# Kernel tuning notes

Measured on AMD Instinct MI355X. Metric: run time of the kernel, lower is better.

Reference implementation:

```python
import jax, jax.numpy as jnp
import numpy as np

B, N, E = 1024, 4096, 16384
MAX_COL_W, ROW_W = 4, 8


def setup_inputs() -> dict:
    key = jax.random.key(0)
    k1, k2, k3, k4, k5 = jax.random.split(key, 5)
    return {
        "channelLLR": jax.random.normal(k1, (B, N), dtype=jnp.float32),
        "e2oLLR": jax.random.normal(k2, (B, E), dtype=jnp.float32),
        "maxColWeight": MAX_COL_W,
        "edgeToVar": jax.random.randint(k3, (B, N, MAX_COL_W), 0, E, dtype=jnp.int32),
        "edgeToVarMask": jnp.ones((B, N, MAX_COL_W), dtype=jnp.float32),
        "oddToEven": jax.random.randint(k4, (B, E), 0, N, dtype=jnp.int32),
        "edgeToChk": jax.random.randint(k5, (B, E, ROW_W - 1), 0, E, dtype=jnp.int32),
        "rowWeight": ROW_W,
        "alpha": jnp.ones((1,), dtype=jnp.float32),
    }


def reference(channelLLR, e2oLLR, maxColWeight, edgeToVar, edgeToVarMask,
              oddToEven, edgeToChk, rowWeight, alpha):
    b = channelLLR.shape[0]
    # variable-node update: gather incoming edge messages, mask, sum
    msgToVars = jnp.take_along_axis(e2oLLR, edgeToVar.reshape(b, -1), axis=1)
    msgToVars = msgToVars.reshape(b, -1, maxColWeight) * edgeToVarMask  # [B,N,colW]
    llr = channelLLR + jnp.sum(msgToVars, axis=2)                      # [B,N]
    # extrinsic variable-to-check message per edge
    llr = jnp.take_along_axis(llr, oddToEven, axis=1) - e2oLLR         # [B,E]
    # check-node min-sum update over rowWeight-1 peer edges
    msgToChecks = jnp.take_along_axis(llr, edgeToChk.reshape(b, -1), axis=1)
    msgToChecks = msgToChecks.reshape(b, -1, rowWeight - 1)            # [B,E,rowW-1]
    mn = jnp.min(jnp.abs(msgToChecks), axis=2)                         # [B,E]
    sign = jnp.prod(jnp.sign(msgToChecks), axis=2)                     # [B,E]
    e2o = sign * (mn * alpha[0])                                       # [B,E]
    # marginalized posterior LLR per variable node
    out = jnp.take_along_axis(e2o, edgeToVar.reshape(b, -1), axis=1)
    out = out.reshape(b, -1, maxColWeight) * edgeToVarMask
    out = channelLLR + jnp.sum(out, axis=2)                            # [B,N]
    return (out, e2o)
```

## Files before the change

kernel.cpp:

```cpp
#include <hip/hip_runtime.h>

#define BB   1024
#define NN   4096
#define EE   16384
#define COLW 4
#define ROWW1 7
#define TPB  512
#define NWAVE (TPB / 64)
#define GRP_DW (64 * ROWW1)
#define NIT  (EE / TPB)

__global__ __launch_bounds__(TPB, 4) void msl_fused_kernel(
    const float* __restrict__ channelLLR,
    const float* __restrict__ e2oLLR,
    const int*   __restrict__ edgeToVar,
    const float* __restrict__ edgeToVarMask,
    const int*   __restrict__ oddToEven,
    const int*   __restrict__ edgeToChk,
    const float* __restrict__ alpha,
    float*       __restrict__ out,
    float*       __restrict__ e2o_out)
{
    __shared__ __align__(16) float scr_lds[NN];
    __shared__ __align__(16) float edge_lds[EE];
    const int b    = blockIdx.x;
    const int tid  = threadIdx.x;
    const int wave = tid >> 6;
    const int lane = tid & 63;
    const float alph = alpha[0];

    {
        const float4* __restrict__ src = reinterpret_cast<const float4*>(e2oLLR + (size_t)b * EE);
        float4* dst = reinterpret_cast<float4*>(edge_lds);
        #pragma unroll
        for (int k = 0; k < EE / 4 / TPB; ++k) {
            int i = tid + k * TPB;
            dst[i] = src[i];
        }
    }
    __syncthreads();

    uint2  idxpk[NN / TPB];
    float4 mreg[NN / TPB];
    {
        const int4*   __restrict__ ev4 = reinterpret_cast<const int4*>(edgeToVar + (size_t)b * NN * COLW);
        const float4* __restrict__ mk4 = reinterpret_cast<const float4*>(edgeToVarMask + (size_t)b * NN * COLW);
        const float*  __restrict__ chrow = channelLLR + (size_t)b * NN;
        #pragma unroll
        for (int k = 0; k < NN / TPB; ++k) {
            int n = tid + k * TPB;
            int4  idx = ev4[n];
            float4 m  = mk4[n];
            float acc = chrow[n];
            acc += edge_lds[idx.x] * m.x;
            acc += edge_lds[idx.y] * m.y;
            acc += edge_lds[idx.z] * m.z;
            acc += edge_lds[idx.w] * m.w;
            scr_lds[n] = acc;
            idxpk[k] = make_uint2((unsigned)idx.x | ((unsigned)idx.y << 16),
                                  (unsigned)idx.z | ((unsigned)idx.w << 16));
            mreg[k] = m;
        }
    }
    __syncthreads();

    {
        const int* __restrict__ o2erow = oddToEven + (size_t)b * EE;
        #pragma unroll 8
        for (int k = 0; k < NIT; ++k) {
            int e = tid + k * TPB;
            edge_lds[e] = scr_lds[o2erow[e]] - edge_lds[e];
        }
    }
    __syncthreads();

    float e2oreg[NIT];
    {
        const int* __restrict__ ecrow = edgeToChk + (size_t)b * (size_t)EE * ROWW1;
        float* __restrict__ e2orow = e2o_out + (size_t)b * EE;
        float* __restrict__ scratch = scr_lds + wave * GRP_DW;
        int idx[ROWW1];
        {
            const int* __restrict__ p = ecrow + (size_t)wave * GRP_DW + lane;
            #pragma unroll
            for (int j = 0; j < ROWW1; ++j) idx[j] = p[64 * j];
        }
        #pragma unroll
        for (int it = 0; it < NIT; ++it) {
            const int g = it * NWAVE + wave;
            __builtin_amdgcn_wave_barrier();
            asm volatile("s_waitcnt lgkmcnt(0)" ::: "memory");
            __builtin_amdgcn_wave_barrier();
            #pragma unroll
            for (int j = 0; j < ROWW1; ++j) scratch[lane + 64 * j] = edge_lds[idx[j]];
            if (it + 1 < NIT) {
                const int* __restrict__ p = ecrow + (size_t)(g + NWAVE) * GRP_DW + lane;
                #pragma unroll
                for (int j = 0; j < ROWW1; ++j) idx[j] = p[64 * j];
            }
            __builtin_amdgcn_wave_barrier();
            asm volatile("s_waitcnt lgkmcnt(0)" ::: "memory");
            __builtin_amdgcn_wave_barrier();
            float mn = 3.0e38f;
            unsigned sgn = 0u;
            const float* __restrict__ sb = scratch + lane * ROWW1;
            #pragma unroll
            for (int j = 0; j < ROWW1; ++j) {
                float u = sb[j];
                sgn ^= __float_as_uint(u);
                mn = fminf(mn, fabsf(u));
            }
            float val = mn * alph;
            float r = __uint_as_float(__float_as_uint(val) ^ (sgn & 0x80000000u));
            e2oreg[it] = r;
            e2orow[64 * g + lane] = r;
        }
    }
    __syncthreads();

    #pragma unroll
    for (int k = 0; k < NIT; ++k) {
        edge_lds[tid + k * TPB] = e2oreg[k];
    }
    __syncthreads();

    {
        float* __restrict__ outrow = out + (size_t)b * NN;
        const float* __restrict__ chrow = channelLLR + (size_t)b * NN;
        #pragma unroll
        for (int k = 0; k < NN / TPB; ++k) {
            int n = tid + k * TPB;
            uint2  pk = idxpk[k];
            float4 m  = mreg[k];
            float acc = chrow[n];
            acc += edge_lds[pk.x & 0xFFFFu] * m.x;
            acc += edge_lds[pk.x >> 16]     * m.y;
            acc += edge_lds[pk.y & 0xFFFFu] * m.z;
            acc += edge_lds[pk.y >> 16]     * m.w;
            outrow[n] = acc;
        }
    }
}

extern "C" void kernel_launch(void* const* d_in, const int* in_sizes, int n_in,
                              void* d_out, int out_size, void* d_ws, size_t ws_size,
                              hipStream_t stream) {
    const float* channelLLR    = (const float*)d_in[0];
    const float* e2oLLR        = (const float*)d_in[1];
    const int*   edgeToVar     = (const int*)d_in[3];
    const float* edgeToVarMask = (const float*)d_in[4];
    const int*   oddToEven     = (const int*)d_in[5];
    const int*   edgeToChk     = (const int*)d_in[6];
    const float* alpha         = (const float*)d_in[8];

    float* out     = (float*)d_out;
    float* e2o_out = (float*)d_out + (size_t)BB * NN;

    msl_fused_kernel<<<BB, TPB, 0, stream>>>(
        channelLLR, e2oLLR, edgeToVar, edgeToVarMask,
        oddToEven, edgeToChk, alpha, out, e2o_out);
}
```

Before: 180.6 us.

## Double block size, stage e2o in separate LDS buffer and write it coalesced

Block size doubles to 1024 threads. A dedicated LDS buffer now holds the check-node outputs, so the register staging and one barrier pass are removed, and e2o is written to global memory as float4 at the end. Edge indices and channel LLRs stay unpacked in registers, so the posterior pass skips the global re-read and the unpacking. LDS use rises to about 156 KB per block, which limits residency to one block per CU and leaves less room to hide barrier stalls.

New measurement: 164.4 us. -9.0%, faster.

```diff
diff --git a/kernel.cpp b/kernel.cpp
--- a/kernel.cpp
+++ b/kernel.cpp
@@ -5,12 +5,13 @@
 #define EE   16384
 #define COLW 4
 #define ROWW1 7
-#define TPB  512
+#define TPB  1024
 #define NWAVE (TPB / 64)
 #define GRP_DW (64 * ROWW1)
+#define SCR_DW (NWAVE * GRP_DW)
 #define NIT  (EE / TPB)
 
-__global__ __launch_bounds__(TPB, 4) void msl_fused_kernel(
+__global__ __launch_bounds__(TPB) void msl_fused_kernel(
     const float* __restrict__ channelLLR,
     const float* __restrict__ e2oLLR,
     const int*   __restrict__ edgeToVar,
@@ -21,8 +22,9 @@
     float*       __restrict__ out,
     float*       __restrict__ e2o_out)
 {
-    __shared__ __align__(16) float scr_lds[NN];
     __shared__ __align__(16) float edge_lds[EE];
+    __shared__ __align__(16) float e2o_lds[EE];
+    __shared__ __align__(16) float scr_lds[SCR_DW];
     const int b    = blockIdx.x;
     const int tid  = threadIdx.x;
     const int wave = tid >> 6;
@@ -40,8 +42,9 @@
     }
     __syncthreads();
 
-    uint2  idxpk[NN / TPB];
+    int4   idxreg[NN / TPB];
     float4 mreg[NN / TPB];
+    float  chreg[NN / TPB];
     {
         const int4*   __restrict__ ev4 = reinterpret_cast<const int4*>(edgeToVar + (size_t)b * NN * COLW);
         const float4* __restrict__ mk4 = reinterpret_cast<const float4*>(edgeToVarMask + (size_t)b * NN * COLW);
@@ -51,15 +54,14 @@
             int n = tid + k * TPB;
             int4  idx = ev4[n];
             float4 m  = mk4[n];
-            float acc = chrow[n];
+            float ch  = chrow[n];
+            float acc = ch;
             acc += edge_lds[idx.x] * m.x;
             acc += edge_lds[idx.y] * m.y;
             acc += edge_lds[idx.z] * m.z;
             acc += edge_lds[idx.w] * m.w;
             scr_lds[n] = acc;
-            idxpk[k] = make_uint2((unsigned)idx.x | ((unsigned)idx.y << 16),
-                                  (unsigned)idx.z | ((unsigned)idx.w << 16));
-            mreg[k] = m;
+            idxreg[k] = idx; mreg[k] = m; chreg[k] = ch;
         }
     }
     __syncthreads();
@@ -74,10 +76,8 @@
     }
     __syncthreads();
 
-    float e2oreg[NIT];
     {
         const int* __restrict__ ecrow = edgeToChk + (size_t)b * (size_t)EE * ROWW1;
-        float* __restrict__ e2orow = e2o_out + (size_t)b * EE;
         float* __restrict__ scratch = scr_lds + wave * GRP_DW;
         int idx[ROWW1];
         {
@@ -112,32 +112,35 @@
             }
             float val = mn * alph;
             float r = __uint_as_float(__float_as_uint(val) ^ (sgn & 0x80000000u));
-            e2oreg[it] = r;
-            e2orow[64 * g + lane] = r;
+            e2o_lds[64 * g + lane] = r;
         }
     }
-    __syncthreads();
 
-    #pragma unroll
-    for (int k = 0; k < NIT; ++k) {
-        edge_lds[tid + k * TPB] = e2oreg[k];
-    }
-    __syncthreads();
+    asm volatile("s_waitcnt lgkmcnt(0)\n\ts_barrier" ::: "memory");
 
     {
         float* __restrict__ outrow = out + (size_t)b * NN;
-        const float* __restrict__ chrow = channelLLR + (size_t)b * NN;
         #pragma unroll
         for (int k = 0; k < NN / TPB; ++k) {
             int n = tid + k * TPB;
-            uint2  pk = idxpk[k];
+            int4  idx = idxreg[k];
             float4 m  = mreg[k];
-            float acc = chrow[n];
-            acc += edge_lds[pk.x & 0xFFFFu] * m.x;
-            acc += edge_lds[pk.x >> 16]     * m.y;
-            acc += edge_lds[pk.y & 0xFFFFu] * m.z;
-            acc += edge_lds[pk.y >> 16]     * m.w;
+            float acc = chreg[k];
+            acc += e2o_lds[idx.x] * m.x;
+            acc += e2o_lds[idx.y] * m.y;
+            acc += e2o_lds[idx.z] * m.z;
+            acc += e2o_lds[idx.w] * m.w;
             outrow[n] = acc;
+        }
+    }
+
+    {
+        const float4* __restrict__ src = reinterpret_cast<const float4*>(e2o_lds);
+        float4* __restrict__ dst = reinterpret_cast<float4*>(e2o_out + (size_t)b * EE);
+        #pragma unroll
+        for (int k = 0; k < EE / 4 / TPB; ++k) {
+            int i = tid + k * TPB;
+            dst[i] = src[i];
         }
     }
 }
```
